# Kernel tuning notes

Measured on AMD Instinct MI355X. Metric: run time of the kernel, lower is better.

## Reference

```python
import jax, jax.numpy as jnp
import numpy as np

N = 50000      # nodes
E = 800000     # edges (avg degree 16)
D = 128        # hidden dim (hidden_dim = [128,128,128])
G = 500        # graphs in batch
NS = 100       # num_stock
M0 = 64        # mid_dim[0] == mid_dim[1]
M2 = 1         # mid_dim[2]
LRELU_SLOPE = 0.2
BN_EPS = 1e-5


def setup_inputs() -> dict:
    key = jax.random.key(0)
    ks = jax.random.split(key, 24)
    s = 0.05
    inp = {
        "x": jax.random.normal(ks[0], (N, D), dtype=jnp.float32),
        "graph_data": jax.random.randint(ks[1], (2, E), 0, N, dtype=jnp.int64)
            if jax.config.read("jax_enable_x64") else jax.random.randint(ks[1], (2, E), 0, N).astype(jnp.int32),
        "batch": jnp.sort(jax.random.randint(ks[2], (N,), 0, G)).astype(jnp.int32),
        # GATv2Conv layer 0 (in=D, out=D, heads=1)
        "wl0": jax.random.normal(ks[3], (D, D)) * s,
        "bl0": jax.random.normal(ks[4], (D,)) * s,
        "wr0": jax.random.normal(ks[5], (D, D)) * s,
        "br0": jax.random.normal(ks[6], (D,)) * s,
        "att0": jax.random.normal(ks[7], (D,)) * s,
        "b0": jax.random.normal(ks[8], (D,)) * s,
        # GATv2Conv layer 1
        "wl1": jax.random.normal(ks[9], (D, D)) * s,
        "bl1": jax.random.normal(ks[10], (D,)) * s,
        "wr1": jax.random.normal(ks[11], (D, D)) * s,
        "br1": jax.random.normal(ks[12], (D,)) * s,
        "att1": jax.random.normal(ks[13], (D,)) * s,
        "b1": jax.random.normal(ks[14], (D,)) * s,
        # BatchNorm1d (eval mode, running stats) applied after layer 0 only
        "bn_gamma": jnp.ones((D,), jnp.float32),
        "bn_beta": jnp.zeros((D,), jnp.float32),
        "bn_mean": jax.random.normal(ks[15], (D,)) * 0.1,
        "bn_var": jax.random.uniform(ks[16], (D,), minval=0.5, maxval=1.5),
        # fc1: hidden_dim[-2] -> num_stock*mid_dim[0]; fc3: mid_dim[1] -> mid_dim[2]
        "fc1_w": jax.random.normal(ks[17], (D, NS * M0)) * s,
        "fc1_b": jax.random.normal(ks[18], (NS * M0,)) * s,
        "fc3_w": jax.random.normal(ks[19], (M0, M2)) * s,
        "fc3_b": jax.random.normal(ks[20], (M2,)) * s,
    }
    return inp


def _gatv2(x, src, dst, wl, bl, wr, br, att, b):
    """PyG GATv2Conv, heads=1, add_self_loops=False, eval mode (no dropout)."""
    xl = x @ wl + bl                      # source-side transform [N, D]
    xr = x @ wr + br                      # target-side transform [N, D]
    # per-edge attention logits: a^T LeakyReLU(x_j + x_i)
    e = jnp.einsum("ed,d->e", jax.nn.leaky_relu(xl[src] + xr[dst], LRELU_SLOPE), att)
    # softmax over incoming edges of each destination node
    m = jax.ops.segment_max(e, dst, num_segments=N)
    m = jnp.where(jnp.isfinite(m), m, 0.0)
    p = jnp.exp(e - m[dst])
    denom = jax.ops.segment_sum(p, dst, num_segments=N)
    alpha = p / denom[dst]
    out = jax.ops.segment_sum(alpha[:, None] * xl[src], dst, num_segments=N)
    return out + b


def reference(x, graph_data, batch, wl0, bl0, wr0, br0, att0, b0,
              wl1, bl1, wr1, br1, att1, b1,
              bn_gamma, bn_beta, bn_mean, bn_var,
              fc1_w, fc1_b, fc3_w, fc3_b):
    src, dst = graph_data[0], graph_data[1]
    # layer 0: GATv2 -> BatchNorm (eval) -> ReLU
    h = _gatv2(x, src, dst, wl0, bl0, wr0, br0, att0, b0)
    h = bn_gamma * (h - bn_mean) * jax.lax.rsqrt(bn_var + BN_EPS) + bn_beta
    h = jax.nn.relu(h)
    # layer 1 (last): GATv2 only
    h = _gatv2(h, src, dst, wl1, bl1, wr1, br1, att1, b1)
    # global mean pool over graphs
    counts = jax.ops.segment_sum(jnp.ones((N,), h.dtype), batch, num_segments=G)
    pooled = jax.ops.segment_sum(h, batch, num_segments=G) / jnp.maximum(counts, 1.0)[:, None]
    # fc1 + reshape to [G, num_stock, mid_dim0]; dropout is eval-mode identity
    h = jax.nn.relu(pooled @ fc1_w + fc1_b).reshape(G, NS, M0)
    out = jax.nn.sigmoid(h @ fc3_w + fc3_b)   # [G, NS, 1]
    return out.reshape(G, NS * M2)
```

## Files before the change

kernel.cpp:

```cpp
#include <hip/hip_runtime.h>

#define DD 128
#define GG 500
#define NSTK 100
#define SLOPE 0.2f
#define BN_EPS 1e-5f
#define XPAD 136
#define SLOT 64
#define LOG2E 1.4426950408889634f
#define NB 196
#define ECAP 5120

typedef __attribute__((ext_vector_type(8))) short bf16x8;
typedef __attribute__((ext_vector_type(4))) float f32x4;
typedef __attribute__((ext_vector_type(2))) float f32x2;
typedef unsigned int uint;
typedef unsigned short ushort;

static __device__ __forceinline__ unsigned short f2bf(float f) {
    union { float f; unsigned int u; } v; v.f = f;
    unsigned int r = (v.u + 0x7fff + ((v.u >> 16) & 1)) >> 16;
    return (unsigned short)r;
}

static __device__ __forceinline__ f32x2 bfpair(uint u) {
    union { uint2 u2; f32x2 f; } c;
    c.u2.x = u << 16;
    c.u2.y = u & 0xffff0000u;
    return c.f;
}

#define ROR_ADD(v, N)                                                              \
    v += __int_as_float(__builtin_amdgcn_update_dpp(                               \
        0, __float_as_int(v), 0x120 + (N), 0xF, 0xF, false))


__global__ __launch_bounds__(128) void wprep_kernel(
    const float* __restrict__ wl0, const float* __restrict__ wr0,
    const float* __restrict__ wl1, const float* __restrict__ wr1,
    unsigned short* __restrict__ wt0, unsigned short* __restrict__ wt1,
    const float* __restrict__ bn_g, const float* __restrict__ bn_b,
    const float* __restrict__ bn_m, const float* __restrict__ bn_v,
    float* __restrict__ bn_scale, float* __restrict__ bn_shift,
    uint* __restrict__ cursor)
{
    int c = blockIdx.x;
    int layer = blockIdx.y;
    int k = threadIdx.x;
    const float* wl = layer ? wl1 : wl0;
    const float* wr = layer ? wr1 : wr0;
    float v = (c < 128) ? wl[k * DD + c] : wr[k * DD + (c - 128)];
    (layer ? wt1 : wt0)[c * DD + k] = f2bf(v);
    if (c == 0 && layer == 0) {
        float s = bn_g[k] * rsqrtf(bn_v[k] + BN_EPS);
        bn_scale[k] = s;
        bn_shift[k] = bn_b[k] - bn_m[k] * s;
    }
    int gid = (blockIdx.y * 256 + blockIdx.x) * 128 + threadIdx.x;
    if (gid < 256) cursor[gid] = 0;
}


__global__ __launch_bounds__(256) void part_mm0_kernel(
    const int* __restrict__ src, const int* __restrict__ dst,
    uint* __restrict__ cursor, uint* __restrict__ ebuf, int e_count, int PB, int MB,
    const float* __restrict__ x, const unsigned short* __restrict__ wt,
    const float* __restrict__ bA, const float* __restrict__ bB,
    unsigned short* __restrict__ outA, unsigned short* __restrict__ outB, int n)
{
    int b = (int)blockIdx.x;
    int L = 2 * (PB < MB ? PB : MB);
    int is_part, id;
    if (b < L)          { is_part = b & 1;        id = b >> 1; }
    else if (PB < MB)   { is_part = 0;            id = b - PB; }
    else                { is_part = 1;            id = b - MB; }

    if (is_part) {
        __shared__ uint hist[256];
        __shared__ uint base[256];
        int t = threadIdx.x;
        hist[t] = 0;
        __syncthreads();

        int e0 = (id * 256 + t) * 8;
        uint bb[8], rk[8], pk[8];
        #pragma unroll
        for (int k = 0; k < 8; ++k) {
            int e = e0 + k;
            if (e < e_count) {
                int d = dst[e];
                int s = src[e];
                uint b_ = (uint)d >> 8;
                bb[k] = b_;
                pk[k] = ((uint)(d & 255) << 16) | (uint)s;
                rk[k] = atomicAdd(&hist[b_], 1u);
            } else bb[k] = 0xFFFFFFFFu;
        }
        __syncthreads();
        if (t < NB) {
            uint h = hist[t];
            base[t] = h ? atomicAdd(&cursor[t], h) : 0u;
        }
        __syncthreads();
        #pragma unroll
        for (int k = 0; k < 8; ++k) {
            if (bb[k] != 0xFFFFFFFFu) {
                uint idx = base[bb[k]] + rk[k];
                if (idx < ECAP) ebuf[bb[k] * ECAP + idx] = pk[k];
            }
        }
        return;
    }

    __shared__ unsigned short xs[32 * XPAD];
    int t = threadIdx.x;
    int row0 = id * 32;

    #pragma unroll
    for (int i = 0; i < 2; ++i) {
        int idx8 = i * 256 + t;
        int r = idx8 >> 4;
        int c = (idx8 & 15) * 8;
        float4 v0 = make_float4(0.f, 0.f, 0.f, 0.f), v1 = v0;
        if (row0 + r < n) {
            v0 = *(const float4*)&x[(size_t)(row0 + r) * DD + c];
            v1 = *(const float4*)&x[(size_t)(row0 + r) * DD + c + 4];
        }
        union { bf16x8 v; unsigned short u[8]; } pk2;
        pk2.u[0] = f2bf(v0.x); pk2.u[1] = f2bf(v0.y); pk2.u[2] = f2bf(v0.z); pk2.u[3] = f2bf(v0.w);
        pk2.u[4] = f2bf(v1.x); pk2.u[5] = f2bf(v1.y); pk2.u[6] = f2bf(v1.z); pk2.u[7] = f2bf(v1.w);
        *(bf16x8*)&xs[r * XPAD + c] = pk2.v;
    }
    __syncthreads();

    int wave = t >> 6, lane = t & 63;
    int m16 = lane & 15;
    int kg = lane >> 4;

    bf16x8 bfr[4][4];
    #pragma unroll
    for (int ct = 0; ct < 4; ++ct) {
        int c = wave * 64 + ct * 16 + m16;
        #pragma unroll
        for (int ks = 0; ks < 4; ++ks)
            bfr[ks][ct] = *(const bf16x8*)&wt[(size_t)c * DD + ks * 32 + kg * 8];
    }

    f32x4 acc[2][4];
    #pragma unroll
    for (int rt = 0; rt < 2; ++rt)
        #pragma unroll
        for (int ct = 0; ct < 4; ++ct) acc[rt][ct] = (f32x4){0.f, 0.f, 0.f, 0.f};

    #pragma unroll
    for (int ks = 0; ks < 4; ++ks) {
        int koff = ks * 32 + kg * 8;
        bf16x8 a[2];
        #pragma unroll
        for (int rt = 0; rt < 2; ++rt)
            a[rt] = *(bf16x8*)&xs[(rt * 16 + m16) * XPAD + koff];
        #pragma unroll
        for (int rt = 0; rt < 2; ++rt)
            #pragma unroll
            for (int ct = 0; ct < 4; ++ct)
                acc[rt][ct] = __builtin_amdgcn_mfma_f32_16x16x32_bf16(a[rt], bfr[ks][ct], acc[rt][ct], 0, 0, 0);
    }

    #pragma unroll
    for (int rt = 0; rt < 2; ++rt) {
        int r0 = row0 + rt * 16 + kg * 4;
        #pragma unroll
        for (int ct = 0; ct < 4; ++ct) {
            int c = wave * 64 + ct * 16 + m16;
            float bb2; unsigned short* op; int cc;
            if (c < 128) { bb2 = bA[c]; op = outA; cc = c; }
            else         { bb2 = bB[c - 128]; op = outB; cc = c - 128; }
            #pragma unroll
            for (int i = 0; i < 4; ++i) {
                if (r0 + i < n)
                    op[(size_t)(r0 + i) * DD + cc] = f2bf(acc[rt][ct][i] + bb2);
            }
        }
    }
}


__global__ __launch_bounds__(256) void build_kernel(
    const uint* __restrict__ ebuf, const uint* __restrict__ cursor,
    ushort* __restrict__ csr, int* __restrict__ deg, int n)
{
    __shared__ int cnt[256];
    int b = blockIdx.x, t = threadIdx.x;
    cnt[t] = 0;
    __syncthreads();
    int total = (int)cursor[b];
    if (total > ECAP) total = ECAP;
    for (int i = t; i < total; i += 256) {
        uint u = ebuf[(size_t)b * ECAP + i];
        int dl = (int)(u >> 16);
        int s  = (int)(u & 0xFFFFu);
        int r = atomicAdd(&cnt[dl], 1);
        if (r < SLOT) csr[(uint)(b * 256 + dl) * 64u + (uint)r] = (ushort)s;
    }
    __syncthreads();
    int node = b * 256 + t;
    if (node < n) {
        int c = cnt[t];
        deg[node] = c < SLOT ? c : SLOT;
    }
}


__global__ __launch_bounds__(256) void gat_agg_kernel(
    const unsigned short* __restrict__ xl, const unsigned short* __restrict__ xr,
    const int* __restrict__ degv, const ushort* __restrict__ csr,
    const float* __restrict__ att, const float* __restrict__ bias,
    const float* __restrict__ bn_scale, const float* __restrict__ bn_shift,
    unsigned short* __restrict__ out_bf, float* __restrict__ out_f32,
    int n, int use_bn)
{
    int wave = (int)((blockIdx.x * 256 + threadIdx.x) >> 6);
    int lane = threadIdx.x & 63;
    if (wave >= n) return;
    int grp = lane >> 4;
    int gl  = lane & 15;
    uint f  = (uint)gl * 8u;

    int csrv = (int)csr[(uint)wave * 64u + (uint)lane];
    int deg = degv[wave];
    if (deg > SLOT) deg = SLOT;

    uint4 xru = *(const uint4*)&xr[(uint)wave * 128u + f];
    f32x2 xrp[4] = {bfpair(xru.x), bfpair(xru.y), bfpair(xru.z), bfpair(xru.w)};
    const f32x2* attp = (const f32x2*)&att[f];
    f32x2 atp[4];
    #pragma unroll
    for (int k = 0; k < 4; ++k) atp[k] = attp[k] * LOG2E;

    f32x2 accp[4] = {{0.f,0.f},{0.f,0.f},{0.f,0.f},{0.f,0.f}};
    float den = 0.f;

    int nIter = (deg + 3) >> 2;
    uint4 au0 = make_uint4(0,0,0,0), au1 = au0;
    {
        int j0 = grp;
        int s0 = __shfl(csrv, j0, 64);
        if (j0 < deg) au0 = *(const uint4*)&xl[(uint)s0 * 128u + f];
        int j1 = grp + 4;
        int s1 = __shfl(csrv, j1, 64);
        if (j1 < deg) au1 = *(const uint4*)&xl[(uint)s1 * 128u + f];
    }

    for (int i = 0; i < nIter; ++i) {
        int j  = grp + i * 4;
        int jn = j + 8;
        int s2 = __shfl(csrv, jn < SLOT ? jn : 0, 64);
        uint4 au2 = make_uint4(0,0,0,0);
        if (jn < deg) au2 = *(const uint4*)&xl[(uint)s2 * 128u + f];

        f32x2 ap[4] = {bfpair(au0.x), bfpair(au0.y), bfpair(au0.z), bfpair(au0.w)};
        f32x2 ld = {0.f, 0.f};
        #pragma unroll
        for (int k = 0; k < 4; ++k) {
            f32x2 tv = ap[k] + xrp[k];
            f32x2 lr = __builtin_elementwise_max(tv, SLOPE * tv);
            ld += atp[k] * lr;
        }
        float partial = ld.x + ld.y;
        ROR_ADD(partial, 1);
        ROR_ADD(partial, 2);
        ROR_ADD(partial, 4);
        ROR_ADD(partial, 8);
        float p = (j < deg) ? exp2f(partial) : 0.f;
        den += p;
        #pragma unroll
        for (int k = 0; k < 4; ++k) accp[k] += p * ap[k];

        au0 = au1; au1 = au2;
    }

    float* accf = (float*)accp;
    #pragma unroll
    for (int k = 0; k < 8; ++k) {
        accf[k] += __shfl_xor(accf[k], 16, 64);
        accf[k] += __shfl_xor(accf[k], 32, 64);
    }
    den += __shfl_xor(den, 16, 64);
    den += __shfl_xor(den, 32, 64);

    if (grp == 0) {
        float inv = (deg > 0) ? 1.0f / den : 0.0f;
        float o[8];
        #pragma unroll
        for (int k = 0; k < 8; ++k) o[k] = accf[k] * inv + bias[f + k];
        if (use_bn) {
            #pragma unroll
            for (int k = 0; k < 8; ++k) {
                o[k] = o[k] * bn_scale[f + k] + bn_shift[f + k];
                o[k] = o[k] > 0.f ? o[k] : 0.f;
            }
        }
        if (out_bf) {
            uint4 pk;
            pk.x = ((uint)f2bf(o[1]) << 16) | f2bf(o[0]);
            pk.y = ((uint)f2bf(o[3]) << 16) | f2bf(o[2]);
            pk.z = ((uint)f2bf(o[5]) << 16) | f2bf(o[4]);
            pk.w = ((uint)f2bf(o[7]) << 16) | f2bf(o[6]);
            *(uint4*)&out_bf[(uint)wave * 128u + f] = pk;
        } else {
            *(float4*)&out_f32[(uint)wave * 128u + f]      = make_float4(o[0], o[1], o[2], o[3]);
            *(float4*)&out_f32[(uint)wave * 128u + f + 4u] = make_float4(o[4], o[5], o[6], o[7]);
        }
    }
}


__global__ __launch_bounds__(256) void dualmm_mfma_kernel(
    const unsigned short* __restrict__ xbf,
    const unsigned short* __restrict__ wt,
    const float* __restrict__ bA, const float* __restrict__ bB,
    unsigned short* __restrict__ outA, unsigned short* __restrict__ outB, int n)
{
    __shared__ unsigned short xs[64 * XPAD];
    __shared__ unsigned short wsh[128 * XPAD];
    int t = threadIdx.x;
    int row0 = blockIdx.x * 64;

    #pragma unroll
    for (int i = 0; i < 4; ++i) {
        int idx = i * 256 + t;
        int r = idx >> 4;
        int c = (idx & 15) * 8;
        uint4 v = make_uint4(0, 0, 0, 0);
        if (row0 + r < n) v = *(const uint4*)&xbf[(size_t)(row0 + r) * DD + c];
        *(uint4*)&xs[r * XPAD + c] = v;
    }

    int wave = t >> 6, lane = t & 63;
    int m16 = lane & 15;
    int kg = lane >> 4;

    for (int half = 0; half < 2; ++half) {
        __syncthreads();
        #pragma unroll
        for (int i = 0; i < 8; ++i) {
            int idx = i * 256 + t;
            int r = idx >> 4;
            int ck = (idx & 15) * 8;
            uint4 v = *(const uint4*)&wt[(size_t)(half * 128 + r) * DD + ck];
            *(uint4*)&wsh[r * XPAD + ck] = v;
        }
        __syncthreads();

        f32x4 acc[4][2];
        #pragma unroll
        for (int rt = 0; rt < 4; ++rt)
            #pragma unroll
            for (int ct = 0; ct < 2; ++ct)
                acc[rt][ct] = (f32x4){0.f, 0.f, 0.f, 0.f};

        #pragma unroll
        for (int ks = 0; ks < 4; ++ks) {
            int koff = ks * 32 + kg * 8;
            bf16x8 a[4], b[2];
            #pragma unroll
            for (int rt = 0; rt < 4; ++rt)
                a[rt] = *(bf16x8*)&xs[(rt * 16 + m16) * XPAD + koff];
            #pragma unroll
            for (int ct = 0; ct < 2; ++ct)
                b[ct] = *(bf16x8*)&wsh[(wave * 32 + ct * 16 + m16) * XPAD + koff];
            #pragma unroll
            for (int rt = 0; rt < 4; ++rt)
                #pragma unroll
                for (int ct = 0; ct < 2; ++ct)
                    acc[rt][ct] = __builtin_amdgcn_mfma_f32_16x16x32_bf16(a[rt], b[ct], acc[rt][ct], 0, 0, 0);
        }

        const float* bias = half ? bB : bA;
        unsigned short* outp = half ? outB : outA;
        #pragma unroll
        for (int rt = 0; rt < 4; ++rt) {
            int r = row0 + rt * 16 + kg * 4;
            #pragma unroll
            for (int ct = 0; ct < 2; ++ct) {
                int c = wave * 32 + ct * 16 + m16;
                float bb = bias[c];
                #pragma unroll
                for (int i = 0; i < 4; ++i) {
                    if (r + i < n)
                        outp[(size_t)(r + i) * DD + c] = f2bf(acc[rt][ct][i] + bb);
                }
            }
        }
    }
}


__device__ __forceinline__ int lower_bound_dev(const int* __restrict__ arr, int n, int val) {
    int lo = 0, hi = n;
    while (lo < hi) {
        int mid = (lo + hi) >> 1;
        if (arr[mid] < val) lo = mid + 1; else hi = mid;
    }
    return lo;
}

__global__ __launch_bounds__(512) void pool_kernel(const float* __restrict__ h,
                                                   const int* __restrict__ batch,
                                                   float* __restrict__ pooled, int n) {
    __shared__ float red[4][DD];
    int g = blockIdx.x;
    int f = threadIdx.x & 127;
    int rg = threadIdx.x >> 7;
    int lo = lower_bound_dev(batch, n, g);
    int hi = lower_bound_dev(batch, n, g + 1);
    float s = 0.f;
    for (int i = lo + rg; i < hi; i += 4) s += h[(size_t)i * DD + f];
    red[rg][f] = s;
    __syncthreads();
    if (rg == 0) {
        float tot = red[0][f] + red[1][f] + red[2][f] + red[3][f];
        float cnt = (float)(hi - lo);
        pooled[(size_t)g * DD + f] = tot / fmaxf(cnt, 1.0f);
    }
}


__global__ __launch_bounds__(64) void head_kernel(
    const float* __restrict__ pooled, const float* __restrict__ fc1_w,
    const float* __restrict__ fc1_b, const float* __restrict__ fc3_w,
    const float* __restrict__ fc3_b, float* __restrict__ out)
{
    int sIdx = blockIdx.x;
    int gbase = blockIdx.y * 20;
    int j = threadIdx.x;

    float wreg[DD];
    #pragma unroll
    for (int k = 0; k < DD; ++k)
        wreg[k] = fc1_w[(size_t)k * (NSTK * 64) + sIdx * 64 + j];
    float b1 = fc1_b[sIdx * 64 + j];
    float w3 = fc3_w[j];
    float b3 = fc3_b[0];

    for (int gi = 0; gi < 20; ++gi) {
        int g = gbase + gi;
        float acc = b1;
        #pragma unroll
        for (int k4 = 0; k4 < DD / 4; ++k4) {
            float4 pv = *(const float4*)&pooled[(size_t)g * DD + k4 * 4];
            acc += pv.x * wreg[k4 * 4 + 0];
            acc += pv.y * wreg[k4 * 4 + 1];
            acc += pv.z * wreg[k4 * 4 + 2];
            acc += pv.w * wreg[k4 * 4 + 3];
        }
        float r = acc > 0.f ? acc : 0.f;
        float v = r * w3;
        #pragma unroll
        for (int off = 32; off; off >>= 1) v += __shfl_xor(v, off, 64);
        if (j == 0) out[(size_t)g * NSTK + sIdx] = 1.0f / (1.0f + __expf(-(v + b3)));
    }
}


extern "C" void kernel_launch(void* const* d_in, const int* in_sizes, int n_in,
                              void* d_out, int out_size, void* d_ws, size_t ws_size,
                              hipStream_t stream) {
    const float* x        = (const float*)d_in[0];
    const int*   graph    = (const int*)d_in[1];
    const int*   batch    = (const int*)d_in[2];
    const float* wl0      = (const float*)d_in[3];
    const float* bl0      = (const float*)d_in[4];
    const float* wr0      = (const float*)d_in[5];
    const float* br0      = (const float*)d_in[6];
    const float* att0     = (const float*)d_in[7];
    const float* b0       = (const float*)d_in[8];
    const float* wl1      = (const float*)d_in[9];
    const float* bl1      = (const float*)d_in[10];
    const float* wr1      = (const float*)d_in[11];
    const float* br1      = (const float*)d_in[12];
    const float* att1     = (const float*)d_in[13];
    const float* b1       = (const float*)d_in[14];
    const float* bn_gamma = (const float*)d_in[15];
    const float* bn_beta  = (const float*)d_in[16];
    const float* bn_mean  = (const float*)d_in[17];
    const float* bn_var   = (const float*)d_in[18];
    const float* fc1_w    = (const float*)d_in[19];
    const float* fc1_b    = (const float*)d_in[20];
    const float* fc3_w    = (const float*)d_in[21];
    const float* fc3_b    = (const float*)d_in[22];
    float* out = (float*)d_out;

    int n       = in_sizes[0] / DD;
    int e_count = in_sizes[1] / 2;
    const int* srcv = graph;
    const int* dstv = graph + e_count;

    unsigned short* A   = (unsigned short*)d_ws;
    unsigned short* B   = A  + (size_t)n * DD;
    unsigned short* Cb  = B  + (size_t)n * DD;
    float* Cf        = (float*)(Cb + (size_t)n * DD);
    float* pooled    = Cf + (size_t)n * DD;
    float* bn_scale  = pooled + (size_t)GG * DD;
    float* bn_shift  = bn_scale + DD;
    int* deg  = (int*)(bn_shift + DD);
    ushort* csr = (ushort*)(deg + n);
    uint* cursor = (uint*)(csr + (size_t)n * SLOT);
    uint* ebuf   = cursor + 256;
    uintptr_t wp = ((uintptr_t)(ebuf + (size_t)NB * ECAP) + 15) & ~(uintptr_t)15;
    unsigned short* wt0 = (unsigned short*)wp;
    unsigned short* wt1 = wt0 + 256 * DD;

    int PB   = ((e_count + 7) / 8 + 255) / 256;
    int MB32 = (n + 31) / 32;

    wprep_kernel<<<dim3(256, 2), 128, 0, stream>>>(wl0, wr0, wl1, wr1, wt0, wt1,
                                                   bn_gamma, bn_beta, bn_mean, bn_var,
                                                   bn_scale, bn_shift, cursor);
    part_mm0_kernel<<<PB + MB32, 256, 0, stream>>>(srcv, dstv, cursor, ebuf, e_count,
                                                   PB, MB32, x, wt0, bl0, br0, A, B, n);
    build_kernel<<<NB, 256, 0, stream>>>(ebuf, cursor, csr, deg, n);
    gat_agg_kernel<<<(n + 3) / 4, 256, 0, stream>>>(A, B, deg, csr, att0, b0,
                                                    bn_scale, bn_shift, Cb, nullptr, n, 1);
    dualmm_mfma_kernel<<<(n + 63) / 64, 256, 0, stream>>>(Cb, wt1, bl1, br1, A, B, n);
    gat_agg_kernel<<<(n + 3) / 4, 256, 0, stream>>>(A, B, deg, csr, att1, b1,
                                                    nullptr, nullptr, nullptr, Cf, n, 0);
    pool_kernel<<<GG, 512, 0, stream>>>(Cf, batch, pooled, n);
    head_kernel<<<dim3(NSTK, GG / 20), 64, 0, stream>>>(pooled, fc1_w, fc1_b, fc3_w, fc3_b, out);
}
```

Baseline: 300.9 us.

## Stage weights in LDS and process 64-row tiles in first-layer matmul

The layer-0 dual matmul in part_mm0 now handles 64 rows per block instead of 32. It stages each 128-column half of the transposed weight matrix into shared memory and loops over the two halves (left/right outputs), instead of each wave loading its weight fragments directly from global memory into registers. This halves the number of matmul blocks and shares each weight load across more rows, at the cost of about 52KB of LDS per block, which lowers occupancy, plus extra barriers. The aggregation kernel's shuffle index clamp is simplified to a bitmask.

Measured after the change: 301.7 us. No clear change (+0.3%).

```diff
diff --git a/kernel.cpp b/kernel.cpp
--- a/kernel.cpp
+++ b/kernel.cpp
@@ -112,12 +112,13 @@
         return;
     }
 
-    __shared__ unsigned short xs[32 * XPAD];
+    __shared__ unsigned short xs[64 * XPAD];
+    __shared__ unsigned short wsh[128 * XPAD];
     int t = threadIdx.x;
-    int row0 = id * 32;
+    int row0 = id * 64;
 
     #pragma unroll
-    for (int i = 0; i < 2; ++i) {
+    for (int i = 0; i < 4; ++i) {
         int idx8 = i * 256 + t;
         int r = idx8 >> 4;
         int c = (idx8 & 15) * 8;
@@ -131,54 +132,62 @@
         pk2.u[4] = f2bf(v1.x); pk2.u[5] = f2bf(v1.y); pk2.u[6] = f2bf(v1.z); pk2.u[7] = f2bf(v1.w);
         *(bf16x8*)&xs[r * XPAD + c] = pk2.v;
     }
-    __syncthreads();
 
     int wave = t >> 6, lane = t & 63;
     int m16 = lane & 15;
     int kg = lane >> 4;
 
-    bf16x8 bfr[4][4];
-    #pragma unroll
-    for (int ct = 0; ct < 4; ++ct) {
-        int c = wave * 64 + ct * 16 + m16;
-        #pragma unroll
-        for (int ks = 0; ks < 4; ++ks)
-            bfr[ks][ct] = *(const bf16x8*)&wt[(size_t)c * DD + ks * 32 + kg * 8];
-    }
-
-    f32x4 acc[2][4];
-    #pragma unroll
-    for (int rt = 0; rt < 2; ++rt)
-        #pragma unroll
-        for (int ct = 0; ct < 4; ++ct) acc[rt][ct] = (f32x4){0.f, 0.f, 0.f, 0.f};
-
-    #pragma unroll
-    for (int ks = 0; ks < 4; ++ks) {
-        int koff = ks * 32 + kg * 8;
-        bf16x8 a[2];
-        #pragma unroll
-        for (int rt = 0; rt < 2; ++rt)
-            a[rt] = *(bf16x8*)&xs[(rt * 16 + m16) * XPAD + koff];
-        #pragma unroll
-        for (int rt = 0; rt < 2; ++rt)
-            #pragma unroll
-            for (int ct = 0; ct < 4; ++ct)
-                acc[rt][ct] = __builtin_amdgcn_mfma_f32_16x16x32_bf16(a[rt], bfr[ks][ct], acc[rt][ct], 0, 0, 0);
-    }
-
-    #pragma unroll
-    for (int rt = 0; rt < 2; ++rt) {
-        int r0 = row0 + rt * 16 + kg * 4;
-        #pragma unroll
-        for (int ct = 0; ct < 4; ++ct) {
-            int c = wave * 64 + ct * 16 + m16;
-            float bb2; unsigned short* op; int cc;
-            if (c < 128) { bb2 = bA[c]; op = outA; cc = c; }
-            else         { bb2 = bB[c - 128]; op = outB; cc = c - 128; }
-            #pragma unroll
-            for (int i = 0; i < 4; ++i) {
-                if (r0 + i < n)
-                    op[(size_t)(r0 + i) * DD + cc] = f2bf(acc[rt][ct][i] + bb2);
+    for (int half = 0; half < 2; ++half) {
+        __syncthreads();
+        #pragma unroll
+        for (int i = 0; i < 8; ++i) {
+            int idx = i * 256 + t;
+            int r = idx >> 4;
+            int ck = (idx & 15) * 8;
+            uint4 v = *(const uint4*)&wt[(size_t)(half * 128 + r) * DD + ck];
+            *(uint4*)&wsh[r * XPAD + ck] = v;
+        }
+        __syncthreads();
+
+        f32x4 acc[4][2];
+        #pragma unroll
+        for (int rt = 0; rt < 4; ++rt)
+            #pragma unroll
+            for (int ct = 0; ct < 2; ++ct)
+                acc[rt][ct] = (f32x4){0.f, 0.f, 0.f, 0.f};
+
+        #pragma unroll
+        for (int ks = 0; ks < 4; ++ks) {
+            int koff = ks * 32 + kg * 8;
+            bf16x8 a[4], bfr[2];
+            #pragma unroll
+            for (int rt = 0; rt < 4; ++rt)
+                a[rt] = *(bf16x8*)&xs[(rt * 16 + m16) * XPAD + koff];
+            #pragma unroll
+            for (int ct = 0; ct < 2; ++ct)
+                bfr[ct] = *(bf16x8*)&wsh[(wave * 32 + ct * 16 + m16) * XPAD + koff];
+            #pragma unroll
+            for (int rt = 0; rt < 4; ++rt)
+                #pragma unroll
+                for (int ct = 0; ct < 2; ++ct)
+                    acc[rt][ct] = __builtin_amdgcn_mfma_f32_16x16x32_bf16(a[rt], bfr[ct], acc[rt][ct], 0, 0, 0);
+        }
+
+        const float* bias = half ? bB : bA;
+        unsigned short* outp = half ? outB : outA;
+        #pragma unroll
+        for (int rt = 0; rt < 4; ++rt) {
+            int r = row0 + rt * 16 + kg * 4;
+            #pragma unroll
+            for (int ct = 0; ct < 2; ++ct) {
+                int c = wave * 32 + ct * 16 + m16;
+                float bb2 = bias[c];
+                unsigned short* op = outp;
+                #pragma unroll
+                for (int i = 0; i < 4; ++i) {
+                    if (r + i < n)
+                        op[(size_t)(r + i) * DD + c] = f2bf(acc[rt][ct][i] + bb2);
+                }
             }
         }
     }
@@ -243,18 +252,16 @@
     int nIter = (deg + 3) >> 2;
     uint4 au0 = make_uint4(0,0,0,0), au1 = au0;
     {
-        int j0 = grp;
-        int s0 = __shfl(csrv, j0, 64);
-        if (j0 < deg) au0 = *(const uint4*)&xl[(uint)s0 * 128u + f];
-        int j1 = grp + 4;
-        int s1 = __shfl(csrv, j1, 64);
-        if (j1 < deg) au1 = *(const uint4*)&xl[(uint)s1 * 128u + f];
+        int s0 = __shfl(csrv, grp, 64);
+        if (grp < deg) au0 = *(const uint4*)&xl[(uint)s0 * 128u + f];
+        int s1 = __shfl(csrv, grp + 4, 64);
+        if (grp + 4 < deg) au1 = *(const uint4*)&xl[(uint)s1 * 128u + f];
     }
 
     for (int i = 0; i < nIter; ++i) {
         int j  = grp + i * 4;
         int jn = j + 8;
-        int s2 = __shfl(csrv, jn < SLOT ? jn : 0, 64);
+        int s2 = __shfl(csrv, jn & 63, 64);
         uint4 au2 = make_uint4(0,0,0,0);
         if (jn < deg) au2 = *(const uint4*)&xl[(uint)s2 * 128u + f];
 
@@ -512,13 +519,13 @@
     unsigned short* wt1 = wt0 + 256 * DD;
 
     int PB   = ((e_count + 7) / 8 + 255) / 256;
-    int MB32 = (n + 31) / 32;
+    int MB64 = (n + 63) / 64;
 
     wprep_kernel<<<dim3(256, 2), 128, 0, stream>>>(wl0, wr0, wl1, wr1, wt0, wt1,
                                                    bn_gamma, bn_beta, bn_mean, bn_var,
                                                    bn_scale, bn_shift, cursor);
-    part_mm0_kernel<<<PB + MB32, 256, 0, stream>>>(srcv, dstv, cursor, ebuf, e_count,
-                                                   PB, MB32, x, wt0, bl0, br0, A, B, n);
+    part_mm0_kernel<<<PB + MB64, 256, 0, stream>>>(srcv, dstv, cursor, ebuf, e_count,
+                                                   PB, MB64, x, wt0, bl0, br0, A, B, n);
     build_kernel<<<NB, 256, 0, stream>>>(ebuf, cursor, csr, deg, n);
     gat_agg_kernel<<<(n + 3) / 4, 256, 0, stream>>>(A, B, deg, csr, att0, b0,
                                                     bn_scale, bn_shift, Cb, nullptr, n, 1);
```
